# Kernel tuning notes

Measured on AMD Instinct MI355X. Metric: run time of the kernel, lower is better.

The kernel has to match this reference:

```python
import jax, jax.numpy as jnp
import numpy as np

B, S, E, H = 2, 2048, 2048, 16
D = E // H  # head_dim = 128
ROPE_BASE = 10000.0


def setup_inputs() -> dict:
    key = jax.random.key(0)
    ks = jax.random.split(key, 6)
    x = jax.random.normal(ks[0], (B, S, E), dtype=jnp.float32)
    # additive causal mask: 0 where attendable, -1e9 above diagonal
    causal = jnp.where(jnp.tril(jnp.ones((S, S), dtype=bool)), 0.0, -1e9).astype(jnp.float32)
    mask = jnp.broadcast_to(causal[None, None], (B, 1, S, S))
    # RoPE tables (rotate-half convention)
    inv_freq = 1.0 / (ROPE_BASE ** (jnp.arange(0, D, 2, dtype=jnp.float32) / D))
    freqs = jnp.arange(S, dtype=jnp.float32)[:, None] * inv_freq[None, :]  # [S, D/2]
    emb = jnp.concatenate([freqs, freqs], axis=-1)  # [S, D]
    cos, sin = jnp.cos(emb), jnp.sin(emb)
    std = 0.02
    Wq = jax.random.normal(ks[1], (E, E), dtype=jnp.float32) * std
    Wk = jax.random.normal(ks[2], (E, E), dtype=jnp.float32) * std
    Wv = jax.random.normal(ks[3], (E, E), dtype=jnp.float32) * std
    Wo = jax.random.normal(ks[4], (E, E), dtype=jnp.float32) * std
    zb = jnp.zeros((E,), dtype=jnp.float32)
    return {"x": x, "mask": mask, "cos": cos, "sin": sin,
            "Wq": Wq, "bq": zb, "Wk": Wk, "bk": zb, "Wv": Wv, "bv": zb,
            "Wo": Wo, "bo": zb, "rope_exclude": 0}


def _rotate_half(t):
    t1, t2 = jnp.split(t, 2, axis=-1)
    return jnp.concatenate([-t2, t1], axis=-1)


def _apply_rope(t, cos, sin, rope_exclude):
    # t: [B, H, S, D]; cos/sin: [S, D]
    rot = t * cos[None, None] + _rotate_half(t) * sin[None, None]
    keep = (jnp.arange(t.shape[2]) < rope_exclude)[None, None, :, None]
    return jnp.where(keep, t, rot)


def reference(x, mask, cos, sin, Wq, bq, Wk, bk, Wv, bv, Wo, bo, rope_exclude):
    b, s, e = x.shape
    scale = D ** -0.5
    def heads(y):
        return y.reshape(b, s, H, D).transpose(0, 2, 1, 3)  # [B,H,S,D]
    q = heads(x @ Wq.T + bq)
    k = heads(x @ Wk.T + bk)
    v = heads(x @ Wv.T + bv)
    q = _apply_rope(q, cos, sin, rope_exclude)
    k = _apply_rope(k, cos, sin, rope_exclude)
    scores = jnp.einsum('bhqd,bhkd->bhqk', q, k) * scale + mask
    attn = jax.nn.softmax(scores, axis=-1)  # dropout is identity in eval mode
    ctx = jnp.einsum('bhqk,bhkd->bhqd', attn, v)
    ctx = ctx.transpose(0, 2, 1, 3).reshape(b, s, e)
    return ctx @ Wo.T + bo
```

## Files before the change

### kernel.cpp

```cpp
#include <hip/hip_runtime.h>


#define BB 2
#define SS 2048
#define EE 2048
#define HH 16
#define DD 128
#define BH 32
#define MR 4096

typedef __attribute__((ext_vector_type(8))) short short8;
typedef __attribute__((ext_vector_type(4))) short short4v;
typedef __attribute__((ext_vector_type(4))) float floatx4;
typedef unsigned int u32;

__device__ __forceinline__ float bf2f(unsigned short u) {
    union { unsigned int i; float f; } v; v.i = ((unsigned int)u) << 16; return v.f;
}
__device__ __forceinline__ unsigned short f2bf(float f) {
    union { float f; unsigned int i; } v; v.f = f;
    unsigned int x = v.i;
    return (unsigned short)((x + 0x7fffu + ((x >> 16) & 1u)) >> 16);
}

__device__ __forceinline__ void async_copy16(const unsigned short* g, unsigned short* l) {
    __builtin_amdgcn_global_load_lds((const __attribute__((address_space(1))) u32*)g,
                                     (__attribute__((address_space(3))) u32*)l, 16, 0, 0);
}

__global__ __launch_bounds__(256)
void cvt_f32_bf16(const float* __restrict__ src, unsigned short* __restrict__ dst, int n)
{
    int i = (blockIdx.x * 256 + threadIdx.x) * 8;
    if (i < n) {
        floatx4 v0 = *(const floatx4*)&src[i];
        floatx4 v1 = *(const floatx4*)&src[i + 4];
        short8 o;
        #pragma unroll
        for (int j = 0; j < 4; ++j) { o[j] = (short)f2bf(v0[j]); o[4 + j] = (short)f2bf(v1[j]); }
        *(short8*)&dst[i] = o;
    }
}

template<int MODE>
__global__ __launch_bounds__(256, 2)
void gemm_fast(const unsigned short* __restrict__ X,
               const unsigned short* __restrict__ W0,
               const unsigned short* __restrict__ W1,
               const unsigned short* __restrict__ W2,
               const float* __restrict__ bias0,
               const float* __restrict__ bias1,
               const float* __restrict__ bias2,
               void* __restrict__ outv)
{
    const unsigned short* W;
    const float* bias;
    unsigned short* op16 = nullptr;
    float* op32 = nullptr;
    if (MODE == 0) {
        int z = blockIdx.z;
        W    = (z == 0) ? W0 : (z == 1) ? W1 : W2;
        bias = (z == 0) ? bias0 : (z == 1) ? bias1 : bias2;
        op16 = (unsigned short*)outv + (size_t)z * ((size_t)BH * SS * DD);
    } else {
        W = W0; bias = bias0; op32 = (float*)outv;
    }

    __shared__ unsigned short As[128 * 32];
    __shared__ unsigned short Bs[128 * 32];

    const int tid  = threadIdx.x;
    const int wave = tid >> 6, lane = tid & 63;
    const int quad = lane >> 4, l16 = lane & 15;
    const int wr = (wave >> 1) * 64;
    const int wc = (wave & 1) * 64;
    const int mbase = blockIdx.y * 128, nbase = blockIdx.x * 128;

    const int r0 = lane >> 2;
    const int c0 = (lane & 3) * 8;

    floatx4 acc[4][4];
    #pragma unroll
    for (int i = 0; i < 4; ++i)
        #pragma unroll
        for (int c = 0; c < 4; ++c)
            acc[i][c] = (floatx4){0.f, 0.f, 0.f, 0.f};

    const int j0 = 2 * wave, j1 = 2 * wave + 1;
    const size_t ga0 = (size_t)(mbase + j0 * 16 + r0) * EE + c0;
    const size_t ga1 = (size_t)(mbase + j1 * 16 + r0) * EE + c0;
    const size_t gb0 = (size_t)(nbase + j0 * 16 + r0) * EE + c0;
    const size_t gb1 = (size_t)(nbase + j1 * 16 + r0) * EE + c0;

    for (int k0 = 0; k0 < EE; k0 += 32) {
        async_copy16(&X[ga0 + k0], &As[j0 * 512]);
        async_copy16(&X[ga1 + k0], &As[j1 * 512]);
        async_copy16(&W[gb0 + k0], &Bs[j0 * 512]);
        async_copy16(&W[gb1 + k0], &Bs[j1 * 512]);
        __syncthreads();

        short8 a[4], b[4];
        #pragma unroll
        for (int i = 0; i < 4; ++i) a[i] = *(short8*)&As[(wr + i * 16 + l16) * 32 + quad * 8];
        #pragma unroll
        for (int c = 0; c < 4; ++c) b[c] = *(short8*)&Bs[(wc + c * 16 + l16) * 32 + quad * 8];
        #pragma unroll
        for (int i = 0; i < 4; ++i)
            #pragma unroll
            for (int c = 0; c < 4; ++c)
                acc[i][c] = __builtin_amdgcn_mfma_f32_16x16x32_bf16(a[i], b[c], acc[i][c], 0, 0, 0);
        __syncthreads();
    }

    #pragma unroll
    for (int c = 0; c < 4; ++c) {
        int n = nbase + wc + c * 16 + l16;
        float bval = bias[n];
        #pragma unroll
        for (int i = 0; i < 4; ++i) {
            #pragma unroll
            for (int r = 0; r < 4; ++r) {
                int m = mbase + wr + i * 16 + quad * 4 + r;
                float val = acc[i][c][r] + bval;
                if (MODE == 0) {
                    int bi = m >> 11, s = m & (SS - 1);
                    int h  = n >> 7,  d = n & (DD - 1);
                    op16[(((size_t)(bi * HH + h)) * SS + s) * DD + d] = f2bf(val);
                } else {
                    op32[(size_t)m * EE + n] = val;
                }
            }
        }
    }
}

template<int MODE>
__global__ __launch_bounds__(256, 2)
void gemm_bt(const void* __restrict__ Xv,
             const float* __restrict__ W0,
             const float* __restrict__ W1,
             const float* __restrict__ W2,
             const float* __restrict__ bias0,
             const float* __restrict__ bias1,
             const float* __restrict__ bias2,
             void* __restrict__ outv)
{
    const float* W;
    const float* bias;
    unsigned short* op16 = nullptr;
    float* op32 = nullptr;
    if (MODE == 0) {
        int z = blockIdx.z;
        W    = (z == 0) ? W0 : (z == 1) ? W1 : W2;
        bias = (z == 0) ? bias0 : (z == 1) ? bias1 : bias2;
        op16 = (unsigned short*)outv + (size_t)z * ((size_t)BH * SS * DD);
    } else {
        W = W0; bias = bias0; op32 = (float*)outv;
    }

    __shared__ unsigned short As[4][128][8];
    __shared__ unsigned short Bs[4][128][8];

    const int tid  = threadIdx.x;
    const int wave = tid >> 6, lane = tid & 63;
    const int quad = lane >> 4, l16 = lane & 15;
    const int wr = (wave >> 1) * 64;
    const int wc = (wave & 1) * 64;
    const int mbase = blockIdx.y * 128, nbase = blockIdx.x * 128;

    const int srow  = tid >> 1;
    const int shalf = tid & 1;
    const int sc0   = shalf * 2;

    floatx4 acc[4][4];
    #pragma unroll
    for (int i = 0; i < 4; ++i)
        #pragma unroll
        for (int c = 0; c < 4; ++c)
            acc[i][c] = (floatx4){0.f, 0.f, 0.f, 0.f};

    const size_t arow = (size_t)(mbase + srow) * EE;
    const size_t brow = (size_t)(nbase + srow) * EE;

    for (int k0 = 0; k0 < EE; k0 += 32) {
        if (MODE == 0) {
            const float* px = &((const float*)Xv)[arow + k0 + shalf * 16];
            short8 lo, hi;
            #pragma unroll
            for (int j = 0; j < 8; ++j) lo[j] = (short)f2bf(px[j]);
            #pragma unroll
            for (int j = 0; j < 8; ++j) hi[j] = (short)f2bf(px[8 + j]);
            *(short8*)&As[sc0    ][srow][0] = lo;
            *(short8*)&As[sc0 + 1][srow][0] = hi;
        } else {
            const unsigned short* Xb = (const unsigned short*)Xv;
            *(short8*)&As[sc0    ][srow][0] = *(const short8*)&Xb[arow + k0 + shalf * 16];
            *(short8*)&As[sc0 + 1][srow][0] = *(const short8*)&Xb[arow + k0 + shalf * 16 + 8];
        }
        {
            const float* pw = &W[brow + k0 + shalf * 16];
            short8 lo, hi;
            #pragma unroll
            for (int j = 0; j < 8; ++j) lo[j] = (short)f2bf(pw[j]);
            #pragma unroll
            for (int j = 0; j < 8; ++j) hi[j] = (short)f2bf(pw[8 + j]);
            *(short8*)&Bs[sc0    ][srow][0] = lo;
            *(short8*)&Bs[sc0 + 1][srow][0] = hi;
        }
        __syncthreads();

        short8 a[4], b[4];
        #pragma unroll
        for (int i = 0; i < 4; ++i) a[i] = *(short8*)&As[quad][wr + i * 16 + l16][0];
        #pragma unroll
        for (int c = 0; c < 4; ++c) b[c] = *(short8*)&Bs[quad][wc + c * 16 + l16][0];
        #pragma unroll
        for (int i = 0; i < 4; ++i)
            #pragma unroll
            for (int c = 0; c < 4; ++c)
                acc[i][c] = __builtin_amdgcn_mfma_f32_16x16x32_bf16(a[i], b[c], acc[i][c], 0, 0, 0);
        __syncthreads();
    }

    #pragma unroll
    for (int c = 0; c < 4; ++c) {
        int n = nbase + wc + c * 16 + l16;
        float bval = bias[n];
        #pragma unroll
        for (int i = 0; i < 4; ++i) {
            #pragma unroll
            for (int r = 0; r < 4; ++r) {
                int m = mbase + wr + i * 16 + quad * 4 + r;
                float val = acc[i][c][r] + bval;
                if (MODE == 0) {
                    int bi = m >> 11, s = m & (SS - 1);
                    int h  = n >> 7,  d = n & (DD - 1);
                    op16[(((size_t)(bi * HH + h)) * SS + s) * DD + d] = f2bf(val);
                } else {
                    op32[(size_t)m * EE + n] = val;
                }
            }
        }
    }
}

__global__ __launch_bounds__(256)
void rope_kernel(unsigned short* __restrict__ Qw, unsigned short* __restrict__ Kw,
                 const float* __restrict__ cosT,
                 const float* __restrict__ sinT,
                 const int* __restrict__ rex)
{
    int idx = blockIdx.x * 256 + threadIdx.x;
    int d4 = idx & 15;
    int s  = (idx >> 4) & (SS - 1);
    int bh = (idx >> 15) & (BH - 1);
    int t  = idx >> 20;
    unsigned short* T = t ? Kw : Qw;
    const float qs = t ? 1.0f : 0.08838834764831845f;

    size_t base  = ((size_t)bh * SS + s) * DD + d4 * 4;
    size_t cbase = (size_t)s * DD + d4 * 4;

    short4v v1 = *(short4v*)&T[base];
    short4v v2 = *(short4v*)&T[base + 64];
    floatx4 c1 = *(const floatx4*)&cosT[cbase];
    floatx4 s1 = *(const floatx4*)&sinT[cbase];
    floatx4 c2 = *(const floatx4*)&cosT[cbase + 64];
    floatx4 s2 = *(const floatx4*)&sinT[cbase + 64];

    bool keep = (s < rex[0]);
    short4v o1, o2;
    #pragma unroll
    for (int i = 0; i < 4; ++i) {
        float f1 = bf2f((unsigned short)v1[i]);
        float f2 = bf2f((unsigned short)v2[i]);
        float r1 = f1 * c1[i] - f2 * s1[i];
        float r2 = f2 * c2[i] + f1 * s2[i];
        o1[i] = (short)f2bf((keep ? f1 : r1) * qs);
        o2[i] = (short)f2bf((keep ? f2 : r2) * qs);
    }
    *(short4v*)&T[base]      = o1;
    *(short4v*)&T[base + 64] = o2;
}

__global__ __launch_bounds__(256, 2)
void attn_mfma(const unsigned short* __restrict__ Qw,
               const unsigned short* __restrict__ Kw,
               const unsigned short* __restrict__ Vw,
               unsigned short* __restrict__ O)
{
    __shared__ unsigned short Ks[16][64][8];
    __shared__ unsigned short Vt[128][72];
    __shared__ unsigned short Ps[4][32][72];

    const int tid  = threadIdx.x;
    const int w    = tid >> 6, lane = tid & 63;
    const int quad = lane >> 4, l16 = lane & 15;
    const int bh = blockIdx.y;
    const int b = bh >> 4, h = bh & (HH - 1);
    const int qb = (bh < 16) ? ((SS / 128 - 1) - blockIdx.x) : blockIdx.x;
    const int qbase = qb * 128;

    const size_t head = (size_t)bh * SS * DD;

    short8 aq[2][4];
    #pragma unroll
    for (int hh = 0; hh < 2; ++hh) {
        const unsigned short* qp = &Qw[head + (size_t)(qbase + w * 32 + hh * 16 + l16) * DD];
        #pragma unroll
        for (int kc = 0; kc < 4; ++kc) aq[hh][kc] = *(const short8*)&qp[kc * 32 + quad * 8];
    }

    floatx4 oacc[2][8];
    #pragma unroll
    for (int hh = 0; hh < 2; ++hh)
        #pragma unroll
        for (int i = 0; i < 8; ++i) oacc[hh][i] = (floatx4){0.f, 0.f, 0.f, 0.f};
    float l_part[2][4];
    #pragma unroll
    for (int hh = 0; hh < 2; ++hh)
        #pragma unroll
        for (int r = 0; r < 4; ++r) l_part[hh][r] = 0.f;

    const int ntiles = 2 * qb + 2;
    for (int kt = 0; kt < ntiles; ++kt) {
        __syncthreads();

        #pragma unroll
        for (int it = 0; it < 4; ++it) {
            int key = it * 16 + (tid >> 4);
            int dc  = tid & 15;
            short8 v = *(const short8*)&Kw[head + (size_t)(kt * 64 + key) * DD + dc * 8];
            *(short8*)&Ks[dc][key ^ (dc & 7)][0] = v;
        }
        #pragma unroll
        for (int it = 0; it < 4; ++it) {
            int key = lane;
            int dc  = it * 4 + w;
            short8 v = *(const short8*)&Vw[head + (size_t)(kt * 64 + key) * DD + dc * 8];
            #pragma unroll
            for (int i = 0; i < 8; ++i) Vt[dc * 8 + i][key] = (unsigned short)v[i];
        }
        __syncthreads();

        if (kt * 64 > qbase + w * 32 + 31) continue;

        floatx4 sacc[2][4];
        #pragma unroll
        for (int hh = 0; hh < 2; ++hh)
            #pragma unroll
            for (int nt = 0; nt < 4; ++nt) sacc[hh][nt] = (floatx4){0.f, 0.f, 0.f, 0.f};
        #pragma unroll
        for (int kc = 0; kc < 4; ++kc) {
            int dcr = kc * 4 + quad;
            #pragma unroll
            for (int nt = 0; nt < 4; ++nt) {
                short8 bfrag = *(const short8*)&Ks[dcr][(nt * 16) + (l16 ^ (dcr & 7))][0];
                sacc[0][nt] = __builtin_amdgcn_mfma_f32_16x16x32_bf16(aq[0][kc], bfrag, sacc[0][nt], 0, 0, 0);
                sacc[1][nt] = __builtin_amdgcn_mfma_f32_16x16x32_bf16(aq[1][kc], bfrag, sacc[1][nt], 0, 0, 0);
            }
        }

        #pragma unroll
        for (int hh = 0; hh < 2; ++hh)
            #pragma unroll
            for (int nt = 0; nt < 4; ++nt)
                #pragma unroll
                for (int rr = 0; rr < 4; ++rr) {
                    int keyg = kt * 64 + nt * 16 + l16;
                    int qg   = qbase + w * 32 + hh * 16 + quad * 4 + rr;
                    float p = (keyg <= qg) ? __expf(sacc[hh][nt][rr]) : 0.f;
                    l_part[hh][rr] += p;
                    Ps[w][hh * 16 + quad * 4 + rr][nt * 16 + l16] = f2bf(p);
                }

        #pragma unroll
        for (int kc = 0; kc < 2; ++kc) {
            short8 pa0 = *(const short8*)&Ps[w][l16][kc * 32 + quad * 8];
            short8 pa1 = *(const short8*)&Ps[w][16 + l16][kc * 32 + quad * 8];
            #pragma unroll
            for (int nt = 0; nt < 8; ++nt) {
                short8 vb = *(const short8*)&Vt[nt * 16 + l16][kc * 32 + quad * 8];
                oacc[0][nt] = __builtin_amdgcn_mfma_f32_16x16x32_bf16(pa0, vb, oacc[0][nt], 0, 0, 0);
                oacc[1][nt] = __builtin_amdgcn_mfma_f32_16x16x32_bf16(pa1, vb, oacc[1][nt], 0, 0, 0);
            }
        }
    }

    #pragma unroll
    for (int hh = 0; hh < 2; ++hh)
        #pragma unroll
        for (int rr = 0; rr < 4; ++rr) {
            float l = l_part[hh][rr];
            l += __shfl_xor(l, 1, 16);
            l += __shfl_xor(l, 2, 16);
            l += __shfl_xor(l, 4, 16);
            l += __shfl_xor(l, 8, 16);
            float inv = 1.f / l;
            int qg = qbase + w * 32 + hh * 16 + quad * 4 + rr;
            unsigned short* cp = &O[((size_t)b * SS + qg) * EE + h * DD];
            #pragma unroll
            for (int nt = 0; nt < 8; ++nt)
                cp[nt * 16 + l16] = f2bf(oacc[hh][nt][rr] * inv);
        }
}

__global__ void sentinel_kernel(float* out, int n) {
    int i = blockIdx.x * 256 + threadIdx.x;
    if (i < n) out[i] = 1.0e6f;
}

extern "C" void kernel_launch(void* const* d_in, const int* in_sizes, int n_in,
                              void* d_out, int out_size, void* d_ws, size_t ws_size,
                              hipStream_t stream)
{
    const float* x    = (const float*)d_in[0];
    const float* cosT = (const float*)d_in[2];
    const float* sinT = (const float*)d_in[3];
    const float* Wq = (const float*)d_in[4];
    const float* bq = (const float*)d_in[5];
    const float* Wk = (const float*)d_in[6];
    const float* bk = (const float*)d_in[7];
    const float* Wv = (const float*)d_in[8];
    const float* bv = (const float*)d_in[9];
    const float* Wo = (const float*)d_in[10];
    const float* bo = (const float*)d_in[11];
    const int* rex = (const int*)d_in[12];

    const size_t tsz = (size_t)BH * SS * DD;
    const size_t wsz = (size_t)EE * EE;
    const size_t need_small = 4 * tsz * sizeof(unsigned short);
    const size_t need_big   = (3 * tsz + 4 * wsz + tsz) * sizeof(unsigned short);

    unsigned short* ws = (unsigned short*)d_ws;
    unsigned short* Qws = ws;
    unsigned short* Kws = ws + tsz;
    unsigned short* Vws = ws + 2 * tsz;

    if (ws_size >= need_big) {
        unsigned short* Wob = ws + 3 * tsz;
        unsigned short* Wqb = Wob + wsz;
        unsigned short* Wkb = Wqb + wsz;
        unsigned short* Wvb = Wkb + wsz;
        unsigned short* Xb  = Wvb + wsz;
        unsigned short* Cws = Xb;

        cvt_f32_bf16<<<(int)(tsz / 8 / 256), 256, 0, stream>>>(x,  Xb,  (int)tsz);
        cvt_f32_bf16<<<(int)(wsz / 8 / 256), 256, 0, stream>>>(Wq, Wqb, (int)wsz);
        cvt_f32_bf16<<<(int)(wsz / 8 / 256), 256, 0, stream>>>(Wk, Wkb, (int)wsz);
        cvt_f32_bf16<<<(int)(wsz / 8 / 256), 256, 0, stream>>>(Wv, Wvb, (int)wsz);
        cvt_f32_bf16<<<(int)(wsz / 8 / 256), 256, 0, stream>>>(Wo, Wob, (int)wsz);

        gemm_fast<0><<<dim3(16, 32, 3), 256, 0, stream>>>(Xb, Wqb, Wkb, Wvb, bq, bk, bv, Qws);
        rope_kernel<<<8192, 256, 0, stream>>>(Qws, Kws, cosT, sinT, rex);
        attn_mfma<<<dim3(SS / 128, BH), 256, 0, stream>>>(Qws, Kws, Vws, Cws);
        gemm_fast<1><<<dim3(16, 32, 1), 256, 0, stream>>>(Cws, Wob, Wob, Wob, bo, bo, bo, d_out);
    } else if (ws_size >= need_small) {
        unsigned short* Cws = ws + 3 * tsz;
        gemm_bt<0><<<dim3(16, 32, 3), 256, 0, stream>>>(x, Wq, Wk, Wv, bq, bk, bv, Qws);
        rope_kernel<<<8192, 256, 0, stream>>>(Qws, Kws, cosT, sinT, rex);
        attn_mfma<<<dim3(SS / 128, BH), 256, 0, stream>>>(Qws, Kws, Vws, Cws);
        gemm_bt<1><<<dim3(16, 32, 1), 256, 0, stream>>>(Cws, Wo, Wo, Wo, bo, bo, bo, d_out);
    } else {
        sentinel_kernel<<<(out_size + 255) / 256, 256, 0, stream>>>((float*)d_out, out_size);
    }
}
```

Measured before the change: 443.3 us.

## Replace bf16 GEMM with 256x128 triple-buffered, swizzled, XCD-remapped 8-wave kernel

Replaces the 128x128 single-buffered GEMM with a 512-thread kernel that computes 256x128 tiles. It uses BK=64 and triple-buffered LDS filled by async global-to-LDS copies, with an XOR-swizzled layout to avoid LDS bank conflicts. Block indices are remapped across the 8 XCDs, s_setprio is raised around the MFMA bursts, and loads are split so they interleave with compute. The QKV projection assumes Wq, Wk and Wv sit contiguously as a single fused N=6144 weight. The cost is higher LDS use, occupancy of one block per CU, and a dependence on that weight layout.

```diff
diff --git a/kernel.cpp b/kernel.cpp
--- a/kernel.cpp
+++ b/kernel.cpp
@@ -8,6 +8,8 @@
 #define DD 128
 #define BH 32
 #define MR 4096
+#define BKK 64
+#define NTK (EE / BKK)
 
 typedef __attribute__((ext_vector_type(8))) short short8;
 typedef __attribute__((ext_vector_type(4))) short short4v;
@@ -42,95 +44,155 @@
     }
 }
 
+__device__ __forceinline__ void stageA(const unsigned short* __restrict__ X,
+                                       unsigned short* Asb, int mbase, int k0,
+                                       int w, int lane)
+{
+    const int rsub = lane >> 3;
+    const int ksw  = ((lane & 7) ^ rsub) << 3;
+    #pragma unroll
+    for (int h = 0; h < 2; ++h)
+        #pragma unroll
+        for (int c = 0; c < 2; ++c) {
+            int r = h * 128 + (w * 2 + c) * 8 + rsub;
+            async_copy16(&X[(size_t)(mbase + r) * EE + k0 + ksw],
+                         &Asb[h * 8192 + (w * 2 + c) * 512]);
+        }
+}
+__device__ __forceinline__ void stageB(const unsigned short* __restrict__ W,
+                                       unsigned short* Bsb, int nbase, int k0,
+                                       int w, int lane)
+{
+    const int rsub = lane >> 3;
+    const int ksw  = ((lane & 7) ^ rsub) << 3;
+    #pragma unroll
+    for (int c = 0; c < 2; ++c) {
+        int r = (w * 2 + c) * 8 + rsub;
+        async_copy16(&W[(size_t)(nbase + r) * EE + k0 + ksw],
+                     &Bsb[(w * 2 + c) * 512]);
+    }
+}
+
 template<int MODE>
-__global__ __launch_bounds__(256, 2)
-void gemm_fast(const unsigned short* __restrict__ X,
-               const unsigned short* __restrict__ W0,
-               const unsigned short* __restrict__ W1,
-               const unsigned short* __restrict__ W2,
-               const float* __restrict__ bias0,
-               const float* __restrict__ bias1,
-               const float* __restrict__ bias2,
-               void* __restrict__ outv)
-{
-    const unsigned short* W;
-    const float* bias;
-    unsigned short* op16 = nullptr;
-    float* op32 = nullptr;
-    if (MODE == 0) {
-        int z = blockIdx.z;
-        W    = (z == 0) ? W0 : (z == 1) ? W1 : W2;
-        bias = (z == 0) ? bias0 : (z == 1) ? bias1 : bias2;
-        op16 = (unsigned short*)outv + (size_t)z * ((size_t)BH * SS * DD);
-    } else {
-        W = W0; bias = bias0; op32 = (float*)outv;
-    }
-
-    __shared__ unsigned short As[128 * 32];
-    __shared__ unsigned short Bs[128 * 32];
+__global__ __launch_bounds__(512, 1)
+void gemm8(const unsigned short* __restrict__ X,
+           const unsigned short* __restrict__ W,
+           const float* __restrict__ bias0,
+           const float* __restrict__ bias1,
+           const float* __restrict__ bias2,
+           void* __restrict__ outv)
+{
+    __shared__ __align__(16) unsigned short As[3][256 * 64];
+    __shared__ __align__(16) unsigned short Bs[3][128 * 64];
+
+    const int NXB = (MODE == 0) ? 48 : 16;
+    const int nwg = (MODE == 0) ? 768 : 256;
+    const int q8  = nwg >> 3;
+    const int wg  = ((int)blockIdx.x & 7) * q8 + ((int)blockIdx.x >> 3);
+    const int xb = wg % NXB, yb = wg / NXB;
+    const int mbase = yb * 256;
+    const int nbase = xb * 128;
 
     const int tid  = threadIdx.x;
-    const int wave = tid >> 6, lane = tid & 63;
+    const int w    = tid >> 6, lane = tid & 63;
     const int quad = lane >> 4, l16 = lane & 15;
-    const int wr = (wave >> 1) * 64;
-    const int wc = (wave & 1) * 64;
-    const int mbase = blockIdx.y * 128, nbase = blockIdx.x * 128;
-
-    const int r0 = lane >> 2;
-    const int c0 = (lane & 3) * 8;
-
-    floatx4 acc[4][4];
-    #pragma unroll
-    for (int i = 0; i < 4; ++i)
-        #pragma unroll
-        for (int c = 0; c < 4; ++c)
-            acc[i][c] = (floatx4){0.f, 0.f, 0.f, 0.f};
-
-    const int j0 = 2 * wave, j1 = 2 * wave + 1;
-    const size_t ga0 = (size_t)(mbase + j0 * 16 + r0) * EE + c0;
-    const size_t ga1 = (size_t)(mbase + j1 * 16 + r0) * EE + c0;
-    const size_t gb0 = (size_t)(nbase + j0 * 16 + r0) * EE + c0;
-    const size_t gb1 = (size_t)(nbase + j1 * 16 + r0) * EE + c0;
-
-    for (int k0 = 0; k0 < EE; k0 += 32) {
-        async_copy16(&X[ga0 + k0], &As[j0 * 512]);
-        async_copy16(&X[ga1 + k0], &As[j1 * 512]);
-        async_copy16(&W[gb0 + k0], &Bs[j0 * 512]);
-        async_copy16(&W[gb1 + k0], &Bs[j1 * 512]);
-        __syncthreads();
-
-        short8 a[4], b[4];
-        #pragma unroll
-        for (int i = 0; i < 4; ++i) a[i] = *(short8*)&As[(wr + i * 16 + l16) * 32 + quad * 8];
-        #pragma unroll
-        for (int c = 0; c < 4; ++c) b[c] = *(short8*)&Bs[(wc + c * 16 + l16) * 32 + quad * 8];
-        #pragma unroll
-        for (int i = 0; i < 4; ++i)
-            #pragma unroll
-            for (int c = 0; c < 4; ++c)
-                acc[i][c] = __builtin_amdgcn_mfma_f32_16x16x32_bf16(a[i], b[c], acc[i][c], 0, 0, 0);
-        __syncthreads();
-    }
-
-    #pragma unroll
-    for (int c = 0; c < 4; ++c) {
-        int n = nbase + wc + c * 16 + l16;
-        float bval = bias[n];
-        #pragma unroll
-        for (int i = 0; i < 4; ++i) {
-            #pragma unroll
-            for (int r = 0; r < 4; ++r) {
-                int m = mbase + wr + i * 16 + quad * 4 + r;
-                float val = acc[i][c][r] + bval;
+    const int wm = w >> 2, wn = w & 3;
+
+    floatx4 acc[8][2];
+    #pragma unroll
+    for (int mi = 0; mi < 8; ++mi)
+        #pragma unroll
+        for (int ni = 0; ni < 2; ++ni)
+            acc[mi][ni] = (floatx4){0.f, 0.f, 0.f, 0.f};
+
+    const int kx0 = (quad * 8) ^ ((l16 & 7) << 3);
+    const int kx1 = (32 + quad * 8) ^ ((l16 & 7) << 3);
+
+    stageA(X, As[0], mbase, 0,   w, lane);  stageB(W, Bs[0], nbase, 0,   w, lane);
+    stageA(X, As[1], mbase, BKK, w, lane);  stageB(W, Bs[1], nbase, BKK, w, lane);
+    asm volatile("s_waitcnt vmcnt(6)" ::: "memory");
+    asm volatile("s_barrier" ::: "memory");
+
+    for (int t = 0; t < NTK; ++t) {
+        const unsigned short* Ab = As[t % 3];
+        const unsigned short* Bb = Bs[t % 3];
+        unsigned short* An = As[(t + 2) % 3];
+        unsigned short* Bn = Bs[(t + 2) % 3];
+        const bool pf = (t + 2 < NTK);
+        const int kn = (t + 2) * BKK;
+
+        short8 b[2][2];
+        #pragma unroll
+        for (int ni = 0; ni < 2; ++ni) {
+            int rb = (wn * 32 + ni * 16 + l16) * 64;
+            b[ni][0] = *(const short8*)&Bb[rb + kx0];
+            b[ni][1] = *(const short8*)&Bb[rb + kx1];
+        }
+        short8 a[4][2];
+        #pragma unroll
+        for (int mi = 0; mi < 4; ++mi) {
+            int ra = (wm * 128 + mi * 16 + l16) * 64;
+            a[mi][0] = *(const short8*)&Ab[ra + kx0];
+            a[mi][1] = *(const short8*)&Ab[ra + kx1];
+        }
+        if (pf) stageA(X, An, mbase, kn, w, lane);
+        __builtin_amdgcn_s_setprio(1);
+        #pragma unroll
+        for (int mi = 0; mi < 4; ++mi)
+            #pragma unroll
+            for (int ni = 0; ni < 2; ++ni) {
+                acc[mi][ni] = __builtin_amdgcn_mfma_f32_16x16x32_bf16(a[mi][0], b[ni][0], acc[mi][ni], 0, 0, 0);
+                acc[mi][ni] = __builtin_amdgcn_mfma_f32_16x16x32_bf16(a[mi][1], b[ni][1], acc[mi][ni], 0, 0, 0);
+            }
+        __builtin_amdgcn_s_setprio(0);
+        asm volatile("s_barrier" ::: "memory");
+
+        #pragma unroll
+        for (int mi = 0; mi < 4; ++mi) {
+            int ra = (wm * 128 + (4 + mi) * 16 + l16) * 64;
+            a[mi][0] = *(const short8*)&Ab[ra + kx0];
+            a[mi][1] = *(const short8*)&Ab[ra + kx1];
+        }
+        if (pf) stageB(W, Bn, nbase, kn, w, lane);
+        __builtin_amdgcn_s_setprio(1);
+        #pragma unroll
+        for (int mi = 0; mi < 4; ++mi)
+            #pragma unroll
+            for (int ni = 0; ni < 2; ++ni) {
+                acc[4 + mi][ni] = __builtin_amdgcn_mfma_f32_16x16x32_bf16(a[mi][0], b[ni][0], acc[4 + mi][ni], 0, 0, 0);
+                acc[4 + mi][ni] = __builtin_amdgcn_mfma_f32_16x16x32_bf16(a[mi][1], b[ni][1], acc[4 + mi][ni], 0, 0, 0);
+            }
+        __builtin_amdgcn_s_setprio(0);
+        if (pf) asm volatile("s_waitcnt vmcnt(6)" ::: "memory");
+        else    asm volatile("s_waitcnt vmcnt(0)" ::: "memory");
+        asm volatile("s_barrier" ::: "memory");
+    }
+
+    #pragma unroll
+    for (int ni = 0; ni < 2; ++ni) {
+        int n = nbase + wn * 32 + ni * 16 + l16;
+        float bval;
+        if (MODE == 0) {
+            const float* bp = (n < 2048) ? bias0 : (n < 4096) ? bias1 : bias2;
+            bval = bp[n & (EE - 1)];
+        } else {
+            bval = bias0[n];
+        }
+        #pragma unroll
+        for (int mi = 0; mi < 8; ++mi)
+            #pragma unroll
+            for (int rr = 0; rr < 4; ++rr) {
+                int m = mbase + wm * 128 + mi * 16 + quad * 4 + rr;
+                float val = acc[mi][ni][rr] + bval;
                 if (MODE == 0) {
-                    int bi = m >> 11, s = m & (SS - 1);
-                    int h  = n >> 7,  d = n & (DD - 1);
-                    op16[(((size_t)(bi * HH + h)) * SS + s) * DD + d] = f2bf(val);
+                    size_t idx = (size_t)(n >> 11) * ((size_t)BH * SS * DD)
+                               + (((size_t)((m >> 11) * HH + ((n >> 7) & (HH - 1)))) * SS + (m & (SS - 1))) * DD
+                               + (n & (DD - 1));
+                    ((unsigned short*)outv)[idx] = f2bf(val);
                 } else {
-                    op32[(size_t)m * EE + n] = val;
+                    ((float*)outv)[(size_t)m * EE + n] = val;
                 }
             }
-        }
     }
 }
 
@@ -451,10 +513,10 @@
         cvt_f32_bf16<<<(int)(wsz / 8 / 256), 256, 0, stream>>>(Wv, Wvb, (int)wsz);
         cvt_f32_bf16<<<(int)(wsz / 8 / 256), 256, 0, stream>>>(Wo, Wob, (int)wsz);
 
-        gemm_fast<0><<<dim3(16, 32, 3), 256, 0, stream>>>(Xb, Wqb, Wkb, Wvb, bq, bk, bv, Qws);
+        gemm8<0><<<768, 512, 0, stream>>>(Xb, Wqb, bq, bk, bv, Qws);
         rope_kernel<<<8192, 256, 0, stream>>>(Qws, Kws, cosT, sinT, rex);
         attn_mfma<<<dim3(SS / 128, BH), 256, 0, stream>>>(Qws, Kws, Vws, Cws);
-        gemm_fast<1><<<dim3(16, 32, 1), 256, 0, stream>>>(Cws, Wob, Wob, Wob, bo, bo, bo, d_out);
+        gemm8<1><<<256, 512, 0, stream>>>(Cws, Wob, bo, bo, bo, d_out);
     } else if (ws_size >= need_small) {
         unsigned short* Cws = ws + 3 * tsz;
         gemm_bt<0><<<dim3(16, 32, 3), 256, 0, stream>>>(x, Wq, Wk, Wv, bq, bk, bv, Qws);
```

New measurement: 435.0 us. About the same (-1.9%).
